# Optimization experiments

Hardware: AMD Instinct MI355X
Metric: run time of the kernel (lower is better)

Reference implementation:

```python
import jax, jax.numpy as jnp
import numpy as np

B, D = 8192, 128


def setup_inputs() -> dict:
    key = jax.random.key(0)
    ks = jax.random.split(key, 7)
    s = 1.0 / np.sqrt(D)  # torch Linear default init scale
    x = jax.random.normal(ks[0], (B, D), jnp.float32)
    W1 = jax.random.uniform(ks[1], (D, D), jnp.float32, -s, s)
    b1 = jax.random.uniform(ks[2], (D,), jnp.float32, -s, s)
    Wmu = jax.random.uniform(ks[3], (D, D), jnp.float32, -s, s)
    bmu = jax.random.uniform(ks[4], (D,), jnp.float32, -s, s)
    Wls = jax.random.uniform(ks[5], (D, D), jnp.float32, -s, s)
    bls = jax.random.uniform(ks[6], (D,), jnp.float32, -s, s)
    return {"x": x, "W1": W1, "b1": b1, "Wmu": Wmu, "bmu": bmu, "Wls": Wls, "bls": bls}


def reference(x, W1, b1, Wmu, bmu, Wls, bls):
    d = x.shape[1]
    mask = jnp.tril(jnp.ones((d, d), x.dtype), -1)  # strict lower triangular, as in MaskedLinear
    W1m = W1 * mask
    Wmum = Wmu * mask
    Wlsm = Wls * mask

    def step(carry, i):
        z, ldj = carry
        h = jax.nn.relu(z @ W1m.T + b1)          # [B, D] hidden (MaskedLinear + ReLU)
        # only column i of mu/logs is consumed each step -> use weight row i
        mu_i = h @ Wmum[i] + bmu[i]              # [B]
        logs_i = h @ Wlsm[i] + bls[i]            # [B]
        z = z.at[:, i].set(mu_i + x[:, i] * jnp.exp(logs_i))
        return (z, ldj + logs_i), None

    z0 = jnp.zeros_like(x)
    ldj0 = jnp.zeros(x.shape[0], x.dtype)
    (z, ldj), _ = jax.lax.scan(step, (z0, ldj0), jnp.arange(d))
    return z, ldj
```

## Files before the change

### kernel.cpp

```cpp
#include <hip/hip_runtime.h>
#include <stdint.h>

#define D 128
#define LOG2E 1.4426950408889634f
#define LN2 0.6931471805599453f

typedef float f2 __attribute__((ext_vector_type(2)));
typedef float f4 __attribute__((ext_vector_type(4)));

__device__ __forceinline__ uint16_t f2bf(float f) {
  uint32_t u = __float_as_uint(f);
  u += 0x7fffu + ((u >> 16) & 1u);
  return (uint16_t)(u >> 16);
}
__device__ __forceinline__ uint32_t pkbf(float a, float b) {
  return (uint32_t)f2bf(a) | ((uint32_t)f2bf(b) << 16);
}
__device__ __forceinline__ f2 unpkbf(uint32_t u) {
  f2 r;
  r.x = __uint_as_float(u << 16);
  r.y = __uint_as_float(u & 0xffff0000u);
  return r;
}
__device__ __forceinline__ float rdlane(float v, int l) {
  return __int_as_float(__builtin_amdgcn_readlane(__float_as_int(v), l));
}
__device__ __forceinline__ float exp2x(float v) {
#if __has_builtin(__builtin_amdgcn_exp2f)
  return __builtin_amdgcn_exp2f(v);
#else
  return exp2f(v);
#endif
}

#define WS_NEED (size_t)(3 * 2048 * 16)

__global__ __launch_bounds__(256)
void iaf_prep(const float* __restrict__ W1, const float* __restrict__ Wmu,
              const float* __restrict__ Wls, uint4* __restrict__ ws) {
  const int t = blockIdx.x * 256 + threadIdx.x;
  if (t >= 32 * 64) return;
  const int jb = t >> 6, l = t & 63;
  const int k0 = 2 * l, k1 = 2 * l + 1;
  uint32_t mm[4], ll[4], ww[4];
#pragma unroll
  for (int c = 0; c < 4; ++c) {
    const int j = jb * 4 + c;
    const float m0 = (j < k0) ? Wmu[k0 * D + j] : 0.f;
    const float m1 = (j < k1) ? Wmu[k1 * D + j] : 0.f;
    const float s0 = (j < k0) ? Wls[k0 * D + j] * LOG2E : 0.f;
    const float s1 = (j < k1) ? Wls[k1 * D + j] * LOG2E : 0.f;
    const float w0 = (j < k0) ? W1[k0 * D + j] : 0.f;
    const float w1_ = (j < k1) ? W1[k1 * D + j] : 0.f;
    mm[c] = pkbf(m0, m1);
    ll[c] = pkbf(s0, s1);
    ww[c] = pkbf(w0, w1_);
  }
  uint4 m4, l4, w4;
  m4.x = mm[0]; m4.y = mm[1]; m4.z = mm[2]; m4.w = mm[3];
  l4.x = ll[0]; l4.y = ll[1]; l4.z = ll[2]; l4.w = ll[3];
  w4.x = ww[0]; w4.y = ww[1]; w4.z = ww[2]; w4.w = ww[3];
  ws[t] = m4;
  ws[2048 + t] = l4;
  ws[4096 + t] = w4;
}

#define SEL(U, c) ((c) == 0 ? (U).x : (c) == 1 ? (U).y : (c) == 2 ? (U).z : (U).w)
#define E(V, c) (((c) & 1) ? (V).y : (V).x)

#define STEP(c, M4, L4, W4, JB)                                     \
  {                                                                 \
    const int Ln = (JB) * 2 + ((c) >> 1);                           \
    const f2 wm = unpkbf(SEL(M4, c));                               \
    const f2 wl = unpkbf(SEL(L4, c));                               \
    const f2 wv = unpkbf(SEL(W4, c));                               \
    const float h = fmaxf(E(pa, c), 0.f);                           \
    const float z = fmaf(E(xR, c), exp2x(E(pls, c)), E(pmu, c));    \
    const float sz = rdlane(z, Ln);                                 \
    const float sh = rdlane(h, Ln);                                 \
    pa = __builtin_elementwise_fma((f2)sz, wv, pa);                 \
    pmu = __builtin_elementwise_fma((f2)sh, wm, pmu);               \
    pls = __builtin_elementwise_fma((f2)sh, wl, pls);               \
  }

__global__ __launch_bounds__(1024, 8)
void iaf_main(const float* __restrict__ x, const float* __restrict__ b1,
              const float* __restrict__ bmu, const float* __restrict__ bls,
              const uint4* __restrict__ ws, float* __restrict__ out, int B) {
  __shared__ uint4 wsh[2 * 2048];

  const int tid = threadIdx.x;
#pragma unroll
  for (int k = 0; k < 4; ++k) wsh[tid + k * 1024] = ws[tid + k * 1024];

  const int lane = tid & 63;
  const int wave = tid >> 6;
  const int row = blockIdx.x * 16 + wave;
  const int l2 = lane * 2;

  const f2 xR = *(const f2*)(x + (size_t)row * D + l2);
  f2 pa = *(const f2*)(b1 + l2);
  f2 pmu = *(const f2*)(bmu + l2);
  f2 pls = *(const f2*)(bls + l2);
  pls.x *= LOG2E;
  pls.y *= LOG2E;

  const uint4* wmuP = wsh + lane;
  const uint4* wlsP = wsh + 2048 + lane;
  const uint4* w1P = ws + 4096 + lane;

  __syncthreads();

  uint4 m0 = wmuP[0], l0 = wlsP[0], w0 = w1P[0];

#pragma unroll 1
  for (int jb = 0; jb < 32; jb += 2) {
    const uint4 m1 = wmuP[64];
    const uint4 l1 = wlsP[64];
    const uint4 w1v = w1P[64];
    STEP(0, m0, l0, w0, jb)
    STEP(1, m0, l0, w0, jb)
    STEP(2, m0, l0, w0, jb)
    STEP(3, m0, l0, w0, jb)
    const int adv = (jb + 2 < 32) ? 128 : 0;
    wmuP += adv;
    wlsP += adv;
    w1P += adv;
    m0 = wmuP[0];
    l0 = wlsP[0];
    w0 = w1P[0];
    STEP(0, m1, l1, w1v, jb + 1)
    STEP(1, m1, l1, w1v, jb + 1)
    STEP(2, m1, l1, w1v, jb + 1)
    STEP(3, m1, l1, w1v, jb + 1)
  }

  f2 zf;
  zf.x = fmaf(xR.x, exp2x(pls.x), pmu.x);
  zf.y = fmaf(xR.y, exp2x(pls.y), pmu.y);
  *(f2*)(out + (size_t)row * D + l2) = zf;

  float ldj = pls.x + pls.y;
#pragma unroll
  for (int m2 = 1; m2 < 64; m2 <<= 1) ldj += __shfl_xor(ldj, m2);
  if (lane == 0) out[(size_t)B * D + row] = ldj * LN2;
}

#define FNTHR 256
#define FRPB 16
#define W1S 136
template <int CTRL>
__device__ __forceinline__ float dppmov(float v) {
  return __int_as_float(
      __builtin_amdgcn_update_dpp(0, __float_as_int(v), CTRL, 0xf, 0xf, true));
}
#define DPP_ADD(v, ctrl) (v) += dppmov<(ctrl)>((v))
__device__ __forceinline__ f2 unpk(uint32_t u) {
  f2 r;
  r.x = __uint_as_float(u << 16);
  r.y = __uint_as_float(u & 0xffff0000u);
  return r;
}
#define RED16F(v)      \
  do {                 \
    DPP_ADD(v, 0xB1);  \
    DPP_ADD(v, 0x4E);  \
    DPP_ADD(v, 0x124); \
    DPP_ADD(v, 0x128); \
  } while (0)
#define FSTEP(I, XE, ZRE, MKE, WM0, WM1, WL0, WL1)                  \
  {                                                                 \
    const float bmu_i = bmu[(I)];                                   \
    const float bls_i = bls[(I)];                                   \
    const f2 h0 = __builtin_elementwise_max(A0, (f2)0.f);           \
    const f2 h1 = __builtin_elementwise_max(A1, (f2)0.f);           \
    const f2 h2_ = __builtin_elementwise_max(A2, (f2)0.f);          \
    const f2 h3 = __builtin_elementwise_max(A3, (f2)0.f);           \
    const f2 q0 = h0 * mk0, q1 = h1 * mk1;                          \
    const f2 q2 = h2_ * mk2, q3 = h3 * mk3;                         \
    f2 am = q0 * WM0.xy;                                            \
    f2 al = q0 * WL0.xy;                                            \
    am = __builtin_elementwise_fma(q1, WM0.zw, am);                 \
    al = __builtin_elementwise_fma(q1, WL0.zw, al);                 \
    am = __builtin_elementwise_fma(q2, WM1.xy, am);                 \
    al = __builtin_elementwise_fma(q2, WL1.xy, al);                 \
    am = __builtin_elementwise_fma(q3, WM1.zw, am);                 \
    al = __builtin_elementwise_fma(q3, WL1.zw, al);                 \
    float mu_p = am.x + am.y;                                       \
    float ls_p = al.x + al.y;                                       \
    {                                                               \
      const int pfr = ((I) + 2 < D) ? (I) + 2 : D - 1;              \
      WM0 = *(const f4*)(wmup + pfr * D);                           \
      WM1 = *(const f4*)(wmup + pfr * D + 4);                       \
      WL0 = *(const f4*)(wlsp + pfr * D);                           \
      WL1 = *(const f4*)(wlsp + pfr * D + 4);                       \
    }                                                               \
    RED16F(mu_p);                                                   \
    RED16F(ls_p);                                                   \
    const float mu_t = mu_p + bmu_i;                                \
    const float ls_t = ls_p + bls_i;                                \
    const float zi = fmaf((XE), __expf(ls_t), mu_t);                \
    ldj += ls_t;                                                    \
    const uint4 wv = *(const uint4*)(w1p + (I)*W1S);                \
    if (own) {                                                      \
      ZRE = zi;                                                     \
      MKE = 1.f;                                                    \
    }                                                               \
    f2 zz;                                                          \
    zz.x = zi;                                                      \
    zz.y = zi;                                                      \
    A0 = __builtin_elementwise_fma(zz, unpk(wv.x), A0);             \
    A1 = __builtin_elementwise_fma(zz, unpk(wv.y), A1);             \
    A2 = __builtin_elementwise_fma(zz, unpk(wv.z), A2);             \
    A3 = __builtin_elementwise_fma(zz, unpk(wv.w), A3);             \
  }

__global__ __launch_bounds__(FNTHR, 2)
void iaf_fb(const float* __restrict__ x, const float* __restrict__ W1,
            const float* __restrict__ b1, const float* __restrict__ Wmu,
            const float* __restrict__ bmu, const float* __restrict__ Wls,
            const float* __restrict__ bls, float* __restrict__ out, int B) {
  __shared__ uint16_t w1c[D * W1S];
  const int tid = threadIdx.x;
  for (int idx = tid; idx < D * D; idx += FNTHR) {
    const int p = idx >> 7, q = idx & (D - 1);
    w1c[q * W1S + p] = f2bf((p > q) ? W1[idx] : 0.f);
  }
  __syncthreads();
  const int lane = tid & 63;
  const int m = lane & 15;
  const int row = blockIdx.x * FRPB + (tid >> 4);
  const float* __restrict__ xp = x + (size_t)row * D;
  const float* __restrict__ wmup = Wmu + m * 8;
  const float* __restrict__ wlsp = Wls + m * 8;
  const uint16_t* __restrict__ w1p = w1c + m * 8;
  f2 A0, A1, A2, A3;
  {
    const f4 t0 = *(const f4*)(b1 + m * 8);
    const f4 t1 = *(const f4*)(b1 + m * 8 + 4);
    A0 = t0.xy; A1 = t0.zw; A2 = t1.xy; A3 = t1.zw;
  }
  f2 mk0 = (f2)0.f, mk1 = (f2)0.f, mk2 = (f2)0.f, mk3 = (f2)0.f;
  float zr0 = 0, zr1 = 0, zr2 = 0, zr3 = 0, zr4 = 0, zr5 = 0, zr6 = 0, zr7 = 0;
  float ldj = 0.f;
  f4 wmA0 = *(const f4*)(wmup);
  f4 wmA1 = *(const f4*)(wmup + 4);
  f4 wlA0 = *(const f4*)(wlsp);
  f4 wlA1 = *(const f4*)(wlsp + 4);
  f4 wmB0 = *(const f4*)(wmup + D);
  f4 wmB1 = *(const f4*)(wmup + D + 4);
  f4 wlB0 = *(const f4*)(wlsp + D);
  f4 wlB1 = *(const f4*)(wlsp + D + 4);
  f4 x4a = *(const f4*)(xp);
  f4 x4b;
  for (int ib = 0; ib < 16; ++ib) {
    const int i0 = ib * 8;
    const bool own = (m == ib);
    x4b = *(const f4*)(xp + i0 + 4);
    FSTEP(i0 + 0, x4a.x, zr0, mk0.x, wmA0, wmA1, wlA0, wlA1);
    FSTEP(i0 + 1, x4a.y, zr1, mk0.y, wmB0, wmB1, wlB0, wlB1);
    FSTEP(i0 + 2, x4a.z, zr2, mk1.x, wmA0, wmA1, wlA0, wlA1);
    FSTEP(i0 + 3, x4a.w, zr3, mk1.y, wmB0, wmB1, wlB0, wlB1);
    {
      const int nx = (i0 + 8 < D) ? i0 + 8 : D - 4;
      x4a = *(const f4*)(xp + nx);
    }
    FSTEP(i0 + 4, x4b.x, zr4, mk2.x, wmA0, wmA1, wlA0, wlA1);
    FSTEP(i0 + 5, x4b.y, zr5, mk2.y, wmB0, wmB1, wlB0, wlB1);
    FSTEP(i0 + 6, x4b.z, zr6, mk3.x, wmA0, wmA1, wlA0, wlA1);
    FSTEP(i0 + 7, x4b.w, zr7, mk3.y, wmB0, wmB1, wlB0, wlB1);
  }
  f4 o0, o1;
  o0.x = zr0; o0.y = zr1; o0.z = zr2; o0.w = zr3;
  o1.x = zr4; o1.y = zr5; o1.z = zr6; o1.w = zr7;
  float* zo = out + (size_t)row * D + m * 8;
  *(f4*)(zo) = o0;
  *(f4*)(zo + 4) = o1;
  if (m == 0) out[(size_t)B * D + row] = ldj;
}

extern "C" void kernel_launch(void* const* d_in, const int* in_sizes, int n_in,
                              void* d_out, int out_size, void* d_ws, size_t ws_size,
                              hipStream_t stream) {
  const float* x   = (const float*)d_in[0];
  const float* W1  = (const float*)d_in[1];
  const float* b1  = (const float*)d_in[2];
  const float* Wmu = (const float*)d_in[3];
  const float* bmu = (const float*)d_in[4];
  const float* Wls = (const float*)d_in[5];
  const float* bls = (const float*)d_in[6];
  float* out = (float*)d_out;

  const int B = in_sizes[0] / D;

  if (ws_size >= WS_NEED) {
    iaf_prep<<<8, 256, 0, stream>>>(W1, Wmu, Wls, (uint4*)d_ws);
    const int grid = (B + 15) / 16;
    iaf_main<<<grid, 1024, 0, stream>>>(x, b1, bmu, bls, (const uint4*)d_ws, out, B);
  } else {
    const int grid = (B + FRPB - 1) / FRPB;
    iaf_fb<<<grid, FNTHR, 0, stream>>>(x, W1, b1, Wmu, bmu, Wls, bls, out, B);
  }
}
```

Baseline: 43.09 us.

## Process eight rows per wave to amortize weight loads across rows

Each wave now carries eight batch rows in registers instead of one, so each unpacked bf16 weight triple is reused eight times and the eight independent rows give ILP to hide readlane/FMA latency. W1 is also moved into shared memory alongside Wmu/Wls. The block shrinks to 256 threads with a 96KB LDS footprint and launch bounds of 1, leaving 256 blocks for 8192 rows. That lowers occupancy and may underfill the GPU's 256 CUs, and register pressure rises.

```diff
diff --git a/kernel.cpp b/kernel.cpp
--- a/kernel.cpp
+++ b/kernel.cpp
@@ -68,46 +68,57 @@
 #define SEL(U, c) ((c) == 0 ? (U).x : (c) == 1 ? (U).y : (c) == 2 ? (U).z : (U).w)
 #define E(V, c) (((c) & 1) ? (V).y : (V).x)
 
-#define STEP(c, M4, L4, W4, JB)                                     \
-  {                                                                 \
-    const int Ln = (JB) * 2 + ((c) >> 1);                           \
-    const f2 wm = unpkbf(SEL(M4, c));                               \
-    const f2 wl = unpkbf(SEL(L4, c));                               \
-    const f2 wv = unpkbf(SEL(W4, c));                               \
-    const float h = fmaxf(E(pa, c), 0.f);                           \
-    const float z = fmaf(E(xR, c), exp2x(E(pls, c)), E(pmu, c));    \
-    const float sz = rdlane(z, Ln);                                 \
-    const float sh = rdlane(h, Ln);                                 \
-    pa = __builtin_elementwise_fma((f2)sz, wv, pa);                 \
-    pmu = __builtin_elementwise_fma((f2)sh, wm, pmu);               \
-    pls = __builtin_elementwise_fma((f2)sh, wl, pls);               \
-  }
-
-__global__ __launch_bounds__(1024, 8)
+#define STEP8(c, M4, L4, W4, JB)                                          \
+  {                                                                       \
+    const int Ln = (JB) * 2 + ((c) >> 1);                                 \
+    const f2 wm = unpkbf(SEL(M4, c));                                     \
+    const f2 wl = unpkbf(SEL(L4, c));                                     \
+    const f2 wv = unpkbf(SEL(W4, c));                                     \
+    _Pragma("unroll") for (int r = 0; r < 8; ++r) {                       \
+      const float h = fmaxf(E(pa[r], c), 0.f);                            \
+      const float z = fmaf(E(xR[r], c), exp2x(E(pls[r], c)), E(pmu[r], c)); \
+      const float sz = rdlane(z, Ln);                                     \
+      const float sh = rdlane(h, Ln);                                     \
+      pa[r] = __builtin_elementwise_fma((f2)sz, wv, pa[r]);               \
+      pmu[r] = __builtin_elementwise_fma((f2)sh, wm, pmu[r]);             \
+      pls[r] = __builtin_elementwise_fma((f2)sh, wl, pls[r]);             \
+    }                                                                     \
+  }
+
+__global__ __launch_bounds__(256, 1)
 void iaf_main(const float* __restrict__ x, const float* __restrict__ b1,
               const float* __restrict__ bmu, const float* __restrict__ bls,
               const uint4* __restrict__ ws, float* __restrict__ out, int B) {
-  __shared__ uint4 wsh[2 * 2048];
+  __shared__ uint4 wsh[3 * 2048];
 
   const int tid = threadIdx.x;
 #pragma unroll
-  for (int k = 0; k < 4; ++k) wsh[tid + k * 1024] = ws[tid + k * 1024];
+  for (int k = 0; k < 24; ++k) wsh[tid + k * 256] = ws[tid + k * 256];
 
   const int lane = tid & 63;
   const int wave = tid >> 6;
-  const int row = blockIdx.x * 16 + wave;
+  const int r0 = blockIdx.x * 32 + wave * 8;
   const int l2 = lane * 2;
 
-  const f2 xR = *(const f2*)(x + (size_t)row * D + l2);
-  f2 pa = *(const f2*)(b1 + l2);
-  f2 pmu = *(const f2*)(bmu + l2);
-  f2 pls = *(const f2*)(bls + l2);
-  pls.x *= LOG2E;
-  pls.y *= LOG2E;
+  f2 xR[8], pa[8], pmu[8], pls[8];
+  {
+    const f2 b1v = *(const f2*)(b1 + l2);
+    const f2 bmv = *(const f2*)(bmu + l2);
+    f2 blv = *(const f2*)(bls + l2);
+    blv.x *= LOG2E;
+    blv.y *= LOG2E;
+#pragma unroll
+    for (int r = 0; r < 8; ++r) {
+      xR[r] = *(const f2*)(x + (size_t)(r0 + r) * D + l2);
+      pa[r] = b1v;
+      pmu[r] = bmv;
+      pls[r] = blv;
+    }
+  }
 
   const uint4* wmuP = wsh + lane;
   const uint4* wlsP = wsh + 2048 + lane;
-  const uint4* w1P = ws + 4096 + lane;
+  const uint4* w1P = wsh + 4096 + lane;
 
   __syncthreads();
 
@@ -118,10 +129,10 @@
     const uint4 m1 = wmuP[64];
     const uint4 l1 = wlsP[64];
     const uint4 w1v = w1P[64];
-    STEP(0, m0, l0, w0, jb)
-    STEP(1, m0, l0, w0, jb)
-    STEP(2, m0, l0, w0, jb)
-    STEP(3, m0, l0, w0, jb)
+    STEP8(0, m0, l0, w0, jb)
+    STEP8(1, m0, l0, w0, jb)
+    STEP8(2, m0, l0, w0, jb)
+    STEP8(3, m0, l0, w0, jb)
     const int adv = (jb + 2 < 32) ? 128 : 0;
     wmuP += adv;
     wlsP += adv;
@@ -129,21 +140,31 @@
     m0 = wmuP[0];
     l0 = wlsP[0];
     w0 = w1P[0];
-    STEP(0, m1, l1, w1v, jb + 1)
-    STEP(1, m1, l1, w1v, jb + 1)
-    STEP(2, m1, l1, w1v, jb + 1)
-    STEP(3, m1, l1, w1v, jb + 1)
-  }
-
-  f2 zf;
-  zf.x = fmaf(xR.x, exp2x(pls.x), pmu.x);
-  zf.y = fmaf(xR.y, exp2x(pls.y), pmu.y);
-  *(f2*)(out + (size_t)row * D + l2) = zf;
-
-  float ldj = pls.x + pls.y;
-#pragma unroll
-  for (int m2 = 1; m2 < 64; m2 <<= 1) ldj += __shfl_xor(ldj, m2);
-  if (lane == 0) out[(size_t)B * D + row] = ldj * LN2;
+    STEP8(0, m1, l1, w1v, jb + 1)
+    STEP8(1, m1, l1, w1v, jb + 1)
+    STEP8(2, m1, l1, w1v, jb + 1)
+    STEP8(3, m1, l1, w1v, jb + 1)
+  }
+
+#pragma unroll
+  for (int r = 0; r < 8; ++r) {
+    f2 zf;
+    zf.x = fmaf(xR[r].x, exp2x(pls[r].x), pmu[r].x);
+    zf.y = fmaf(xR[r].y, exp2x(pls[r].y), pmu[r].y);
+    *(f2*)(out + (size_t)(r0 + r) * D + l2) = zf;
+  }
+  float ldj[8];
+#pragma unroll
+  for (int r = 0; r < 8; ++r) ldj[r] = pls[r].x + pls[r].y;
+#pragma unroll
+  for (int m2 = 1; m2 < 64; m2 <<= 1) {
+#pragma unroll
+    for (int r = 0; r < 8; ++r) ldj[r] += __shfl_xor(ldj[r], m2);
+  }
+  if (lane == 0) {
+#pragma unroll
+    for (int r = 0; r < 8; ++r) out[(size_t)B * D + r0 + r] = ldj[r] * LN2;
+  }
 }
 
 #define FNTHR 256
@@ -295,8 +316,8 @@
 
   if (ws_size >= WS_NEED) {
     iaf_prep<<<8, 256, 0, stream>>>(W1, Wmu, Wls, (uint4*)d_ws);
-    const int grid = (B + 15) / 16;
-    iaf_main<<<grid, 1024, 0, stream>>>(x, b1, bmu, bls, (const uint4*)d_ws, out, B);
+    const int grid = (B + 31) / 32;
+    iaf_main<<<grid, 256, 0, stream>>>(x, b1, bmu, bls, (const uint4*)d_ws, out, B);
   } else {
     const int grid = (B + FRPB - 1) / FRPB;
     iaf_fb<<<grid, FNTHR, 0, stream>>>(x, W1, b1, Wmu, bmu, Wls, bls, out, B);
```

Measured after the change: 36.41 us. 1.18x faster.
